# Kernel optimization log

Measured on AMD Instinct MI355X. Metric: run time of the kernel, lower is better.

Reference implementation:

```python
import jax, jax.numpy as jnp
import numpy as np

# Uniform-scope sizes: B molecules, A atoms/mol, G fragments/mol, W map width,
# H hidden, L attention layers, S = G+1 (fg prompt row prepended per molecule)
B, A, G, W, H, L = 1024, 64, 31, 8, 512, 2
S = G + 1
DK = 32  # attention head dim (hard-coded in the module)


def _layernorm(x, g, b, eps):
    mu = jnp.mean(x, axis=-1, keepdims=True)
    var = jnp.var(x, axis=-1, keepdims=True)
    return g * (x - mu) * jax.lax.rsqrt(var + eps) + b


def setup_inputs() -> dict:
    key = jax.random.key(0)
    ks = jax.random.split(key, 16)
    s = 0.02
    return {
        "f_atom": jax.random.normal(ks[0], (B * A, H), jnp.float32),
        "f_group": jax.random.normal(ks[1], (B * G, H), jnp.float32),
        "fg": jax.random.normal(ks[2], (1, 3 * H), jnp.float32),
        "alpha": 0.1 * jnp.ones((1,), jnp.float32),
        "lr_w": jax.random.normal(ks[3], (3 * H, H), jnp.float32) * s,
        "lr_b": jnp.zeros((H,), jnp.float32),
        "wq_w": jax.random.normal(ks[4], (L, H, DK), jnp.float32) * s,
        "wq_b": jnp.zeros((L, DK), jnp.float32),
        "wk_w": jax.random.normal(ks[5], (L, H, DK), jnp.float32) * s,
        "wk_b": jnp.zeros((L, DK), jnp.float32),
        "wv_w": jax.random.normal(ks[6], (L, H, DK), jnp.float32) * s,
        "wv_b": jnp.zeros((L, DK), jnp.float32),
        "dense_w": jax.random.normal(ks[7], (L, DK, H), jnp.float32) * s,
        "dense_b": jnp.zeros((L, H), jnp.float32),
        "ln_g": jnp.ones((L, H), jnp.float32),
        "ln_b": jnp.zeros((L, H), jnp.float32),
        "lin_w": jax.random.normal(ks[8], (H, H), jnp.float32) * s,
        "lin_b": jnp.zeros((H,), jnp.float32),
        "norm_g": jnp.ones((H,), jnp.float32),
        "norm_b": jnp.zeros((H,), jnp.float32),
        "mapping": jax.random.randint(ks[9], (B * G, W), 0, A + 1, jnp.int64),
    }


def reference(f_atom, f_group, fg, alpha, lr_w, lr_b, wq_w, wq_b, wk_w, wk_b,
              wv_w, wv_b, dense_w, dense_b, ln_g, ln_b, lin_w, lin_b,
              norm_g, norm_b, mapping):
    # --- ragged gather + reduce + pad (vectorized: uniform scopes) ---
    a = f_atom.reshape(B, A, H)
    # prepend zero padding row per molecule (mapping index 0 -> zeros)
    a_pad = jnp.concatenate([jnp.zeros((B, 1, H), a.dtype), a], axis=1)  # [B,A+1,H]
    m = mapping.reshape(B, G, W)
    gathered = a_pad[jnp.arange(B)[:, None, None], m]  # [B,G,W,H]
    g = f_group.reshape(B, G, H)
    cur_g = jnp.concatenate(
        [gathered.sum(axis=2), gathered.max(axis=2), g], axis=-1)  # [B,G,3H]
    brics = jnp.concatenate(
        [jnp.broadcast_to(fg[None], (B, 1, 3 * H)), cur_g], axis=1)  # [B,S,3H]

    f_frag = jax.nn.relu(brics @ lr_w + lr_b)  # [B,S,H]

    # mask built from init_hiddens = f_frag (same for every layer)
    pm = (f_frag != 0).astype(f_frag.dtype)
    mask = jnp.einsum('bsh,bth->bst', pm, pm)  # [B,S,S]
    neg = jnp.asarray(-1e9, f_frag.dtype)
    scale = 1.0 / np.sqrt(DK)

    hs = f_frag
    attn = None
    for l in range(L):
        q = hs @ wq_w[l] + wq_b[l]
        k = hs @ wk_w[l] + wk_b[l]
        v = hs @ wv_w[l] + wv_b[l]
        scores = jnp.einsum('bsd,btd->bst', q, k) * scale
        scores = jnp.where(mask == 0, neg, scores)
        attn = jax.nn.softmax(scores, axis=-1)
        x = jnp.einsum('bst,btd->bsd', attn, v)
        dh = x @ dense_w[l] + dense_b[l]  # dropout is identity in eval
        hs = _layernorm(dh + hs, ln_g[l], ln_b[l], 1e-6)

    f_out = _layernorm(hs @ lin_w + lin_b, norm_g, norm_b, 1e-5) * alpha[0]
    return f_out[:, 0, :], attn
```

## Files before the change

### kernel.cpp

```cpp
#include <hip/hip_runtime.h>

#define B_   1024
#define A_   64
#define G_   31
#define W_   8
#define H_   512
#define L_   2
#define S_   32
#define DK_  32
#define K3H_ 1536

typedef short short8 __attribute__((ext_vector_type(8)));
typedef float floatx4 __attribute__((ext_vector_type(4)));

__device__ __forceinline__ float bf2f(unsigned short u){
  union { unsigned int i; float f; } x; x.i = ((unsigned int)u) << 16; return x.f;
}
__device__ __forceinline__ unsigned short f2bf(float f){
  union { float f; unsigned int i; } x; x.f = f;
  unsigned int u = x.i;
  return (unsigned short)((u + 0x7FFFu + ((u >> 16) & 1u)) >> 16);
}
__device__ __forceinline__ void gl_lds16(const unsigned short* g, unsigned short* l){
  __builtin_amdgcn_global_load_lds((const __attribute__((address_space(1))) unsigned int*)g,
                                   (__attribute__((address_space(3))) unsigned int*)l, 16, 0, 0);
}

__global__ __launch_bounds__(256) void prep_weights(
    const float* __restrict__ lr_w, const float* __restrict__ wq_w, const float* __restrict__ wk_w,
    const float* __restrict__ wv_w, const float* __restrict__ dense_w, const float* __restrict__ lin_w,
    unsigned short* __restrict__ lr_wT, unsigned short* __restrict__ qkvT,
    unsigned short* __restrict__ denseT, unsigned short* __restrict__ lin_wT){
  int i = blockIdx.x * 256 + threadIdx.x;
  if (i < 786432){
    int n = i / K3H_, k = i % K3H_;
    lr_wT[i] = f2bf(lr_w[(size_t)k * H_ + n]);
    return;
  }
  i -= 786432;
  if (i < 98304){
    int k = i & 511; int t = i >> 9; int n = t & 31; int u = t >> 5;
    int p = u % 3, l = u / 3;
    const float* src = (p == 0) ? wq_w : (p == 1) ? wk_w : wv_w;
    qkvT[((size_t)((l*3+p)*S_ + n)) * H_ + k] = f2bf(src[((size_t)(l*H_ + k)) * DK_ + n]);
    return;
  }
  i -= 98304;
  if (i < 32768){
    int k = i & 31; int t = i >> 5; int n = t & 511; int l = t >> 9;
    denseT[((size_t)(l*H_ + n)) * DK_ + k] = f2bf(dense_w[((size_t)(l*DK_ + k)) * H_ + n]);
    return;
  }
  i -= 32768;
  int n = i >> 9, k = i & 511;
  lin_wT[(size_t)n * H_ + k] = f2bf(lin_w[(size_t)k * H_ + n]);
}

__global__ __launch_bounds__(64) void build_brics(
    const float* __restrict__ f_atom, const float* __restrict__ f_group,
    const float* __restrict__ fg, const int* __restrict__ mapping,
    unsigned short* __restrict__ brics){
  int blk = blockIdx.x;
  int b = blk >> 5, s = blk & 31;
  int t = threadIdx.x;
  unsigned short* out = brics + (size_t)blk * K3H_;
  if (s == 0){
    for (int k = t; k < K3H_; k += 64) out[k] = f2bf(fg[k]);
    return;
  }
  int g = s - 1;
  const int* mp = mapping + ((size_t)(b * G_ + g)) * W_;
  int c0 = t * 8;
  float sum[8], mx[8];
  #pragma unroll
  for (int j = 0; j < 8; ++j){ sum[j] = 0.f; mx[j] = -3.4e38f; }
  for (int w = 0; w < W_; ++w){
    int idx = mp[w];
    if (idx == 0){
      #pragma unroll
      for (int j = 0; j < 8; ++j) mx[j] = fmaxf(mx[j], 0.f);
    } else {
      const float* row = f_atom + ((size_t)(b * A_ + idx - 1)) * H_ + c0;
      float4 v0 = *(const float4*)row;
      float4 v1 = *(const float4*)(row + 4);
      float v[8] = {v0.x,v0.y,v0.z,v0.w,v1.x,v1.y,v1.z,v1.w};
      #pragma unroll
      for (int j = 0; j < 8; ++j){ sum[j] += v[j]; mx[j] = fmaxf(mx[j], v[j]); }
    }
  }
  const float* grow = f_group + ((size_t)(b * G_ + g)) * H_ + c0;
  float4 g0 = *(const float4*)grow;
  float4 g1 = *(const float4*)(grow + 4);
  float gv[8] = {g0.x,g0.y,g0.z,g0.w,g1.x,g1.y,g1.z,g1.w};
  unsigned short tmp[8] __attribute__((aligned(16)));
  #pragma unroll
  for (int j = 0; j < 8; ++j) tmp[j] = f2bf(sum[j]);
  *(uint4*)(out + c0) = *(const uint4*)tmp;
  #pragma unroll
  for (int j = 0; j < 8; ++j) tmp[j] = f2bf(mx[j]);
  *(uint4*)(out + 512 + c0) = *(const uint4*)tmp;
  #pragma unroll
  for (int j = 0; j < 8; ++j) tmp[j] = f2bf(gv[j]);
  *(uint4*)(out + 1024 + c0) = *(const uint4*)tmp;
}

__global__ __launch_bounds__(256) void gemm_frag(
    const unsigned short* __restrict__ brics, const unsigned short* __restrict__ wT,
    const float* __restrict__ lr_b, unsigned short* __restrict__ f_frag){
  __shared__ __align__(16) unsigned short As[128*32];
  __shared__ __align__(16) unsigned short Bs[128*32];
  int tid = threadIdx.x;
  int bx = blockIdx.x;
  int mtile = bx >> 2, ntile = bx & 3;
  int rowStart = mtile * 128, colStart = ntile * 128;
  int lane = tid & 63, wave = tid >> 6;
  int m16 = lane & 15, quad = lane >> 4;
  int wm = wave >> 1, wn = wave & 1;
  floatx4 acc[4][4];
  #pragma unroll
  for (int i = 0; i < 4; ++i)
    #pragma unroll
    for (int j = 0; j < 4; ++j) acc[i][j] = (floatx4){0.f,0.f,0.f,0.f};

  int r0 = tid >> 2, c0 = tid & 3;
  int r1 = (tid + 256) >> 2;
  for (int kt = 0; kt < K3H_/32; ++kt){
    const unsigned short* gA0 = brics + (size_t)(rowStart + r0) * K3H_ + kt*32 + c0*8;
    const unsigned short* gA1 = brics + (size_t)(rowStart + r1) * K3H_ + kt*32 + c0*8;
    const unsigned short* gB0 = wT + (size_t)(colStart + r0) * K3H_ + kt*32 + c0*8;
    const unsigned short* gB1 = wT + (size_t)(colStart + r1) * K3H_ + kt*32 + c0*8;
    gl_lds16(gA0, As + (size_t)tid * 8);
    gl_lds16(gA1, As + (size_t)(tid + 256) * 8);
    gl_lds16(gB0, Bs + (size_t)tid * 8);
    gl_lds16(gB1, Bs + (size_t)(tid + 256) * 8);
    __syncthreads();
    short8 af[4], bfr[4];
    #pragma unroll
    for (int i = 0; i < 4; ++i){
      af[i]  = *(const short8*)(As + ((wm*64 + i*16 + m16)*32 + quad*8));
      bfr[i] = *(const short8*)(Bs + ((wn*64 + i*16 + m16)*32 + quad*8));
    }
    #pragma unroll
    for (int i = 0; i < 4; ++i)
      #pragma unroll
      for (int j = 0; j < 4; ++j)
        acc[i][j] = __builtin_amdgcn_mfma_f32_16x16x32_bf16(af[i], bfr[j], acc[i][j], 0, 0, 0);
    __syncthreads();
  }
  #pragma unroll
  for (int i = 0; i < 4; ++i)
    #pragma unroll
    for (int j = 0; j < 4; ++j){
      int col = colStart + wn*64 + j*16 + m16;
      float bias = lr_b[col];
      #pragma unroll
      for (int r = 0; r < 4; ++r){
        int row = rowStart + wm*64 + i*16 + quad*4 + r;
        float v = acc[i][j][r] + bias;
        v = v > 0.f ? v : 0.f;
        f_frag[(size_t)row * H_ + col] = f2bf(v);
      }
    }
}

__global__ __launch_bounds__(256) void attn_kernel(
    const unsigned short* __restrict__ f_frag,
    const unsigned short* __restrict__ qkvT, const unsigned short* __restrict__ denseT,
    const float* __restrict__ wq_b, const float* __restrict__ wk_b, const float* __restrict__ wv_b,
    const float* __restrict__ dense_b, const float* __restrict__ ln_g, const float* __restrict__ ln_b,
    unsigned short* __restrict__ hsf, float* __restrict__ out_attn){
  const int HP = 544, TP = 40;
  __shared__ __align__(16) unsigned short hs[S_*544];
  __shared__ __align__(16) unsigned short Qs[S_*40];
  __shared__ __align__(16) unsigned short Ks[S_*40];
  __shared__ __align__(16) unsigned short Vt[S_*40];
  __shared__ __align__(16) unsigned short Ps[S_*40];
  __shared__ __align__(16) unsigned short Xs[S_*40];
  __shared__ unsigned long long pmask[S_*8];
  __shared__ unsigned int mz[S_];
  int b = blockIdx.x;
  int tid = threadIdx.x;
  int wave = tid >> 6, lane = tid & 63;
  int m16 = lane & 15, quad = lane >> 4;

  {
    int row = tid >> 3, cc = (tid & 7) * 64;
    const unsigned short* src = f_frag + ((size_t)(b * S_ + row)) * H_ + cc;
    unsigned short* dst = hs + row * HP + cc;
    #pragma unroll
    for (int k = 0; k < 64; k += 8)
      *(uint4*)(dst + k) = *(const uint4*)(src + k);
  }
  if (tid < S_) mz[tid] = 0u;
  __syncthreads();
  {
    int s = tid >> 3, w = tid & 7;
    unsigned long long m = 0ull;
    const unsigned short* hrow = hs + s * HP + w * 64;
    for (int j = 0; j < 64; ++j)
      if (hrow[j] != 0) m |= (1ull << j);
    pmask[s * 8 + w] = m;
  }
  __syncthreads();
  for (int idx = tid; idx < S_*S_; idx += 256){
    int s = idx >> 5, t2 = idx & 31;
    bool inter = false;
    #pragma unroll
    for (int w = 0; w < 8; ++w)
      inter = inter || ((pmask[s*8+w] & pmask[t2*8+w]) != 0ull);
    if (!inter) atomicOr(&mz[s], 1u << t2);
  }
  __syncthreads();

  const float scale = 0.17677669529663687f;
  for (int l = 0; l < L_; ++l){
    {
      int mt = wave >> 1, nt = wave & 1;
      floatx4 aq = {0,0,0,0}, ak = {0,0,0,0}, av = {0,0,0,0};
      const unsigned short* arow = hs + (mt*16 + m16) * HP + quad*8;
      const unsigned short* bq = qkvT + ((size_t)((l*3 + 0)*S_ + nt*16 + m16)) * H_ + quad*8;
      const unsigned short* bk = bq + (size_t)S_ * H_;
      const unsigned short* bv = bk + (size_t)S_ * H_;
      for (int k0 = 0; k0 < H_; k0 += 32){
        short8 a = *(const short8*)(arow + k0);
        aq = __builtin_amdgcn_mfma_f32_16x16x32_bf16(a, *(const short8*)(bq + k0), aq, 0,0,0);
        ak = __builtin_amdgcn_mfma_f32_16x16x32_bf16(a, *(const short8*)(bk + k0), ak, 0,0,0);
        av = __builtin_amdgcn_mfma_f32_16x16x32_bf16(a, *(const short8*)(bv + k0), av, 0,0,0);
      }
      int col = nt*16 + m16;
      float bqs = wq_b[l*DK_ + col], bks = wk_b[l*DK_ + col], bvs = wv_b[l*DK_ + col];
      #pragma unroll
      for (int r = 0; r < 4; ++r){
        int rw = mt*16 + quad*4 + r;
        Qs[rw*TP + col] = f2bf((aq[r] + bqs) * scale);
        Ks[rw*TP + col] = f2bf(ak[r] + bks);
        Vt[col*TP + rw] = f2bf(av[r] + bvs);
      }
    }
    __syncthreads();
    if (wave < 2){
      int mt = wave;
      short8 a  = *(const short8*)(Qs + (mt*16 + m16)*TP + quad*8);
      short8 b0 = *(const short8*)(Ks + m16*TP + quad*8);
      short8 b1 = *(const short8*)(Ks + (16 + m16)*TP + quad*8);
      floatx4 z = {0,0,0,0};
      floatx4 s0 = __builtin_amdgcn_mfma_f32_16x16x32_bf16(a, b0, z, 0,0,0);
      floatx4 s1 = __builtin_amdgcn_mfma_f32_16x16x32_bf16(a, b1, z, 0,0,0);
      #pragma unroll
      for (int r = 0; r < 4; ++r){
        int s = mt*16 + quad*4 + r;
        unsigned int m = mz[s];
        float v0 = ((m >> m16) & 1u) ? -1e9f : s0[r];
        float v1 = ((m >> (16 + m16)) & 1u) ? -1e9f : s1[r];
        float mx = fmaxf(v0, v1);
        #pragma unroll
        for (int d = 1; d < 16; d <<= 1) mx = fmaxf(mx, __shfl_xor(mx, d));
        float e0 = __expf(v0 - mx), e1 = __expf(v1 - mx);
        float sm = e0 + e1;
        #pragma unroll
        for (int d = 1; d < 16; d <<= 1) sm += __shfl_xor(sm, d);
        float inv = 1.f / sm;
        float p0 = e0 * inv, p1 = e1 * inv;
        Ps[s*TP + m16] = f2bf(p0);
        Ps[s*TP + 16 + m16] = f2bf(p1);
        if (l == L_ - 1){
          float* oa = out_attn + ((size_t)b * S_ + s) * S_;
          oa[m16] = p0; oa[16 + m16] = p1;
        }
      }
    }
    __syncthreads();
    {
      int mt = wave >> 1, nt = wave & 1;
      short8 a  = *(const short8*)(Ps + (mt*16 + m16)*TP + quad*8);
      short8 bv = *(const short8*)(Vt + (nt*16 + m16)*TP + quad*8);
      floatx4 z = {0,0,0,0};
      floatx4 x = __builtin_amdgcn_mfma_f32_16x16x32_bf16(a, bv, z, 0,0,0);
      #pragma unroll
      for (int r = 0; r < 4; ++r)
        Xs[(mt*16 + quad*4 + r)*TP + nt*16 + m16] = f2bf(x[r]);
    }
    __syncthreads();
    {
      short8 ax0 = *(const short8*)(Xs + m16*TP + quad*8);
      short8 ax1 = *(const short8*)(Xs + (16 + m16)*TP + quad*8);
      #pragma unroll
      for (int j = 0; j < 8; ++j){
        int col = (wave*8 + j)*16 + m16;
        short8 bw = *(const short8*)(denseT + ((size_t)(l*H_ + col)) * DK_ + quad*8);
        float db = dense_b[l*H_ + col];
        floatx4 z = {0,0,0,0};
        floatx4 d0 = __builtin_amdgcn_mfma_f32_16x16x32_bf16(ax0, bw, z, 0,0,0);
        floatx4 d1 = __builtin_amdgcn_mfma_f32_16x16x32_bf16(ax1, bw, z, 0,0,0);
        #pragma unroll
        for (int r = 0; r < 4; ++r){
          int row0 = quad*4 + r;
          float y0 = d0[r] + db + bf2f(hs[row0*HP + col]);
          hs[row0*HP + col] = f2bf(y0);
          int row1 = 16 + quad*4 + r;
          float y1 = d1[r] + db + bf2f(hs[row1*HP + col]);
          hs[row1*HP + col] = f2bf(y1);
        }
      }
    }
    __syncthreads();
    {
      #pragma unroll
      for (int rr = 0; rr < 8; ++rr){
        int row = wave*8 + rr;
        unsigned short* hrow = hs + row*HP + lane*8;
        short8 hv = *(const short8*)hrow;
        float v[8]; float s1 = 0.f, s2 = 0.f;
        #pragma unroll
        for (int j = 0; j < 8; ++j){ v[j] = bf2f((unsigned short)hv[j]); s1 += v[j]; s2 += v[j]*v[j]; }
        #pragma unroll
        for (int d = 1; d < 64; d <<= 1){ s1 += __shfl_xor(s1, d); s2 += __shfl_xor(s2, d); }
        float mean = s1 * (1.f/512.f);
        float var = s2 * (1.f/512.f) - mean*mean;
        float rs = rsqrtf(var + 1e-6f);
        unsigned short o[8] __attribute__((aligned(16)));
        #pragma unroll
        for (int j = 0; j < 8; ++j){
          int colj = lane*8 + j;
          float nv = (v[j] - mean) * rs * ln_g[l*H_ + colj] + ln_b[l*H_ + colj];
          o[j] = f2bf(nv);
        }
        *(uint4*)hrow = *(const uint4*)o;
      }
    }
    __syncthreads();
  }
  if (tid < 64){
    *(uint4*)(hsf + (size_t)b * H_ + tid*8) = *(const uint4*)(hs + tid*8);
  }
}

__global__ __launch_bounds__(256) void final_kernel(
    const unsigned short* __restrict__ hsf, const unsigned short* __restrict__ lin_wT,
    const float* __restrict__ lin_b, const float* __restrict__ norm_g, const float* __restrict__ norm_b,
    const float* __restrict__ alpha, float* __restrict__ out_f){
  const int HP = 544;
  __shared__ __align__(16) unsigned short hsb[32*544];
  int blk = blockIdx.x;
  int tid = threadIdx.x;
  int wave = tid >> 6, lane = tid & 63;
  int m16 = lane & 15, quad = lane >> 4;
  {
    int row = tid >> 3, cc = (tid & 7) * 64;
    const unsigned short* src = hsf + ((size_t)(blk*32 + row)) * H_ + cc;
    unsigned short* dst = hsb + row*HP + cc;
    #pragma unroll
    for (int k = 0; k < 64; k += 8)
      *(uint4*)(dst + k) = *(const uint4*)(src + k);
  }
  __syncthreads();
  floatx4 acc[2][8];
  #pragma unroll
  for (int mt = 0; mt < 2; ++mt)
    #pragma unroll
    for (int j = 0; j < 8; ++j) acc[mt][j] = (floatx4){0.f,0.f,0.f,0.f};
  for (int k0 = 0; k0 < H_; k0 += 32){
    short8 a0 = *(const short8*)(hsb + m16*HP + k0 + quad*8);
    short8 a1 = *(const short8*)(hsb + (16 + m16)*HP + k0 + quad*8);
    #pragma unroll
    for (int j = 0; j < 8; ++j){
      int n = (wave*8 + j)*16 + m16;
      short8 bw = *(const short8*)(lin_wT + (size_t)n * H_ + k0 + quad*8);
      acc[0][j] = __builtin_amdgcn_mfma_f32_16x16x32_bf16(a0, bw, acc[0][j], 0,0,0);
      acc[1][j] = __builtin_amdgcn_mfma_f32_16x16x32_bf16(a1, bw, acc[1][j], 0,0,0);
    }
  }
  __syncthreads();
  #pragma unroll
  for (int mt = 0; mt < 2; ++mt)
    #pragma unroll
    for (int j = 0; j < 8; ++j){
      int col = (wave*8 + j)*16 + m16;
      float lb = lin_b[col];
      #pragma unroll
      for (int r = 0; r < 4; ++r){
        int row = mt*16 + quad*4 + r;
        hsb[row*HP + col] = f2bf(acc[mt][j][r] + lb);
      }
    }
  __syncthreads();
  float al = alpha[0];
  #pragma unroll
  for (int rr = 0; rr < 8; ++rr){
    int row = wave*8 + rr;
    const unsigned short* hrow = hsb + row*HP + lane*8;
    short8 hv = *(const short8*)hrow;
    float v[8]; float s1 = 0.f, s2 = 0.f;
    #pragma unroll
    for (int j = 0; j < 8; ++j){ v[j] = bf2f((unsigned short)hv[j]); s1 += v[j]; s2 += v[j]*v[j]; }
    #pragma unroll
    for (int d = 1; d < 64; d <<= 1){ s1 += __shfl_xor(s1, d); s2 += __shfl_xor(s2, d); }
    float mean = s1 * (1.f/512.f);
    float var = s2 * (1.f/512.f) - mean*mean;
    float rs = rsqrtf(var + 1e-5f);
    float o[8];
    #pragma unroll
    for (int j = 0; j < 8; ++j){
      int colj = lane*8 + j;
      o[j] = ((v[j] - mean) * rs * norm_g[colj] + norm_b[colj]) * al;
    }
    float* op = out_f + ((size_t)(blk*32 + row)) * H_ + lane*8;
    float4 f0 = {o[0], o[1], o[2], o[3]};
    float4 f1 = {o[4], o[5], o[6], o[7]};
    *(float4*)op = f0;
    *(float4*)(op + 4) = f1;
  }
}

extern "C" void kernel_launch(void* const* d_in, const int* in_sizes, int n_in,
                              void* d_out, int out_size, void* d_ws, size_t ws_size,
                              hipStream_t stream){
  const float* f_atom  = (const float*)d_in[0];
  const float* f_group = (const float*)d_in[1];
  const float* fg      = (const float*)d_in[2];
  const float* alpha   = (const float*)d_in[3];
  const float* lr_w    = (const float*)d_in[4];
  const float* lr_b    = (const float*)d_in[5];
  const float* wq_w    = (const float*)d_in[6];
  const float* wq_b    = (const float*)d_in[7];
  const float* wk_w    = (const float*)d_in[8];
  const float* wk_b    = (const float*)d_in[9];
  const float* wv_w    = (const float*)d_in[10];
  const float* wv_b    = (const float*)d_in[11];
  const float* dense_w = (const float*)d_in[12];
  const float* dense_b = (const float*)d_in[13];
  const float* ln_g    = (const float*)d_in[14];
  const float* ln_b    = (const float*)d_in[15];
  const float* lin_w   = (const float*)d_in[16];
  const float* lin_b   = (const float*)d_in[17];
  const float* norm_g  = (const float*)d_in[18];
  const float* norm_b  = (const float*)d_in[19];
  const int*   mapping = (const int*)d_in[20];

  unsigned short* brics  = (unsigned short*)d_ws;
  unsigned short* f_frag = brics  + (size_t)32768 * 1536;
  unsigned short* lr_wT  = f_frag + (size_t)32768 * 512;
  unsigned short* qkvT   = lr_wT  + (size_t)512 * 1536;
  unsigned short* denseT = qkvT   + (size_t)2*3*32*512;
  unsigned short* lin_wT = denseT + (size_t)2*512*32;
  unsigned short* hsf    = lin_wT + (size_t)512*512;

  float* out_f    = (float*)d_out;
  float* out_attn = out_f + (size_t)B_ * H_;

  prep_weights<<<4608, 256, 0, stream>>>(lr_w, wq_w, wk_w, wv_w, dense_w, lin_w,
                                         lr_wT, qkvT, denseT, lin_wT);
  build_brics<<<B_ * S_, 64, 0, stream>>>(f_atom, f_group, fg, mapping, brics);
  gemm_frag<<<(32768/128) * (512/128), 256, 0, stream>>>(brics, lr_wT, lr_b, f_frag);
  attn_kernel<<<B_, 256, 0, stream>>>(f_frag, qkvT, denseT, wq_b, wk_b, wv_b,
                                      dense_b, ln_g, ln_b, hsf, out_attn);
  final_kernel<<<B_/32, 256, 0, stream>>>(hsf, lin_wT, lin_b, norm_g, norm_b, alpha, out_f);
}
```

Baseline: 514.5 us.

## Tile weight transposes, widen brics blocks, and swizzle gemm_frag LDS with K=64

Splits weight prep into an LDS-tiled transpose kernel for the large lr_w/lin_w matrices, which gives coalesced reads and writes, and a small kernel for the qkv/dense weights. build_brics now packs four (molecule, row) pairs into one 256-thread block. gemm_frag doubles its K step to 64 with an XOR-swizzled LDS layout to avoid bank conflicts and halve the number of barriers. It also remaps block IDs so that blocks sharing an M tile land on the same XCD for L2 reuse. The cost is more LDS per block, which could lower occupancy.

```diff
diff --git a/kernel.cpp b/kernel.cpp
--- a/kernel.cpp
+++ b/kernel.cpp
@@ -26,18 +26,41 @@
                                    (__attribute__((address_space(3))) unsigned int*)l, 16, 0, 0);
 }
 
-__global__ __launch_bounds__(256) void prep_weights(
-    const float* __restrict__ lr_w, const float* __restrict__ wq_w, const float* __restrict__ wk_w,
-    const float* __restrict__ wv_w, const float* __restrict__ dense_w, const float* __restrict__ lin_w,
-    unsigned short* __restrict__ lr_wT, unsigned short* __restrict__ qkvT,
-    unsigned short* __restrict__ denseT, unsigned short* __restrict__ lin_wT){
+__global__ __launch_bounds__(256) void prep_transpose(
+    const float* __restrict__ lr_w, const float* __restrict__ lin_w,
+    unsigned short* __restrict__ lr_wT, unsigned short* __restrict__ lin_wT){
+  __shared__ float tile[64][65];
+  int bx = blockIdx.x;
+  const float* src; unsigned short* dst; int R, C;
+  if (bx < 192){ src = lr_w;  dst = lr_wT;  R = 1536; C = 512; }
+  else         { bx -= 192; src = lin_w; dst = lin_wT; R = 512;  C = 512; }
+  int rt = bx >> 3, ct = bx & 7;
+  int tid = threadIdx.x;
+  int r16 = tid >> 4, c4 = tid & 15;
+  #pragma unroll
+  for (int p = 0; p < 4; ++p){
+    int row = p*16 + r16;
+    float4 v = *(const float4*)(src + (size_t)(rt*64 + row) * C + ct*64 + c4*4);
+    tile[row][c4*4+0] = v.x; tile[row][c4*4+1] = v.y;
+    tile[row][c4*4+2] = v.z; tile[row][c4*4+3] = v.w;
+  }
+  __syncthreads();
+  int rr = tid >> 3, cc8 = tid & 7;
+  #pragma unroll
+  for (int p = 0; p < 2; ++p){
+    int n = p*32 + rr;
+    unsigned short o[8] __attribute__((aligned(16)));
+    #pragma unroll
+    for (int j = 0; j < 8; ++j) o[j] = f2bf(tile[cc8*8 + j][n]);
+    *(uint4*)(dst + (size_t)(ct*64 + n) * R + rt*64 + cc8*8) = *(const uint4*)o;
+  }
+}
+
+__global__ __launch_bounds__(256) void prep_small(
+    const float* __restrict__ wq_w, const float* __restrict__ wk_w, const float* __restrict__ wv_w,
+    const float* __restrict__ dense_w,
+    unsigned short* __restrict__ qkvT, unsigned short* __restrict__ denseT){
   int i = blockIdx.x * 256 + threadIdx.x;
-  if (i < 786432){
-    int n = i / K3H_, k = i % K3H_;
-    lr_wT[i] = f2bf(lr_w[(size_t)k * H_ + n]);
-    return;
-  }
-  i -= 786432;
   if (i < 98304){
     int k = i & 511; int t = i >> 9; int n = t & 31; int u = t >> 5;
     int p = u % 3, l = u / 3;
@@ -46,24 +69,18 @@
     return;
   }
   i -= 98304;
-  if (i < 32768){
-    int k = i & 31; int t = i >> 5; int n = t & 511; int l = t >> 9;
-    denseT[((size_t)(l*H_ + n)) * DK_ + k] = f2bf(dense_w[((size_t)(l*DK_ + k)) * H_ + n]);
-    return;
-  }
-  i -= 32768;
-  int n = i >> 9, k = i & 511;
-  lin_wT[(size_t)n * H_ + k] = f2bf(lin_w[(size_t)k * H_ + n]);
-}
-
-__global__ __launch_bounds__(64) void build_brics(
+  int k = i & 31; int t = i >> 5; int n = t & 511; int l = t >> 9;
+  denseT[((size_t)(l*H_ + n)) * DK_ + k] = f2bf(dense_w[((size_t)(l*DK_ + k)) * H_ + n]);
+}
+
+__global__ __launch_bounds__(256) void build_brics(
     const float* __restrict__ f_atom, const float* __restrict__ f_group,
     const float* __restrict__ fg, const int* __restrict__ mapping,
     unsigned short* __restrict__ brics){
-  int blk = blockIdx.x;
-  int b = blk >> 5, s = blk & 31;
-  int t = threadIdx.x;
-  unsigned short* out = brics + (size_t)blk * K3H_;
+  int pair = blockIdx.x * 4 + (threadIdx.x >> 6);
+  int b = pair >> 5, s = pair & 31;
+  int t = threadIdx.x & 63;
+  unsigned short* out = brics + (size_t)pair * K3H_;
   if (s == 0){
     for (int k = t; k < K3H_; k += 64) out[k] = f2bf(fg[k]);
     return;
@@ -107,11 +124,13 @@
 __global__ __launch_bounds__(256) void gemm_frag(
     const unsigned short* __restrict__ brics, const unsigned short* __restrict__ wT,
     const float* __restrict__ lr_b, unsigned short* __restrict__ f_frag){
-  __shared__ __align__(16) unsigned short As[128*32];
-  __shared__ __align__(16) unsigned short Bs[128*32];
+  __shared__ __align__(16) unsigned short As[128*64];
+  __shared__ __align__(16) unsigned short Bs[128*64];
   int tid = threadIdx.x;
   int bx = blockIdx.x;
-  int mtile = bx >> 2, ntile = bx & 3;
+  int xcd = bx & 7, slot = bx >> 3;
+  int mtile = xcd + 8 * (slot >> 2);
+  int ntile = slot & 3;
   int rowStart = mtile * 128, colStart = ntile * 128;
   int lane = tid & 63, wave = tid >> 6;
   int m16 = lane & 15, quad = lane >> 4;
@@ -122,29 +141,40 @@
     #pragma unroll
     for (int j = 0; j < 4; ++j) acc[i][j] = (floatx4){0.f,0.f,0.f,0.f};
 
-  int r0 = tid >> 2, c0 = tid & 3;
-  int r1 = (tid + 256) >> 2;
-  for (int kt = 0; kt < K3H_/32; ++kt){
-    const unsigned short* gA0 = brics + (size_t)(rowStart + r0) * K3H_ + kt*32 + c0*8;
-    const unsigned short* gA1 = brics + (size_t)(rowStart + r1) * K3H_ + kt*32 + c0*8;
-    const unsigned short* gB0 = wT + (size_t)(colStart + r0) * K3H_ + kt*32 + c0*8;
-    const unsigned short* gB1 = wT + (size_t)(colStart + r1) * K3H_ + kt*32 + c0*8;
-    gl_lds16(gA0, As + (size_t)tid * 8);
-    gl_lds16(gA1, As + (size_t)(tid + 256) * 8);
-    gl_lds16(gB0, Bs + (size_t)tid * 8);
-    gl_lds16(gB1, Bs + (size_t)(tid + 256) * 8);
-    __syncthreads();
-    short8 af[4], bfr[4];
-    #pragma unroll
-    for (int i = 0; i < 4; ++i){
-      af[i]  = *(const short8*)(As + ((wm*64 + i*16 + m16)*32 + quad*8));
-      bfr[i] = *(const short8*)(Bs + ((wn*64 + i*16 + m16)*32 + quad*8));
-    }
-    #pragma unroll
-    for (int i = 0; i < 4; ++i)
-      #pragma unroll
-      for (int j = 0; j < 4; ++j)
-        acc[i][j] = __builtin_amdgcn_mfma_f32_16x16x32_bf16(af[i], bfr[j], acc[i][j], 0, 0, 0);
+  int srow = tid >> 3;
+  int gchunk = (tid & 7) ^ (srow & 7);
+  size_t aOff[4], bOff[4];
+  #pragma unroll
+  for (int p = 0; p < 4; ++p){
+    aOff[p] = (size_t)(rowStart + p*32 + srow) * K3H_ + gchunk*8;
+    bOff[p] = (size_t)(colStart + p*32 + srow) * K3H_ + gchunk*8;
+  }
+  int fsw0 = ((0*4 + quad) ^ (m16 & 7)) * 8;
+  int fsw1 = ((1*4 + quad) ^ (m16 & 7)) * 8;
+
+  for (int kt = 0; kt < K3H_/64; ++kt){
+    int kbase = kt * 64;
+    #pragma unroll
+    for (int p = 0; p < 4; ++p){
+      gl_lds16(brics + aOff[p] + kbase, As + p*2048 + (size_t)tid*8);
+      gl_lds16(wT    + bOff[p] + kbase, Bs + p*2048 + (size_t)tid*8);
+    }
+    __syncthreads();
+    #pragma unroll
+    for (int ks = 0; ks < 2; ++ks){
+      int fsw = ks ? fsw1 : fsw0;
+      short8 af[4], bfr[4];
+      #pragma unroll
+      for (int i = 0; i < 4; ++i){
+        af[i]  = *(const short8*)(As + (wm*64 + i*16 + m16)*64 + fsw);
+        bfr[i] = *(const short8*)(Bs + (wn*64 + i*16 + m16)*64 + fsw);
+      }
+      #pragma unroll
+      for (int i = 0; i < 4; ++i)
+        #pragma unroll
+        for (int j = 0; j < 4; ++j)
+          acc[i][j] = __builtin_amdgcn_mfma_f32_16x16x32_bf16(af[i], bfr[j], acc[i][j], 0, 0, 0);
+    }
     __syncthreads();
   }
   #pragma unroll
@@ -448,9 +478,9 @@
   float* out_f    = (float*)d_out;
   float* out_attn = out_f + (size_t)B_ * H_;
 
-  prep_weights<<<4608, 256, 0, stream>>>(lr_w, wq_w, wk_w, wv_w, dense_w, lin_w,
-                                         lr_wT, qkvT, denseT, lin_wT);
-  build_brics<<<B_ * S_, 64, 0, stream>>>(f_atom, f_group, fg, mapping, brics);
+  prep_transpose<<<256, 256, 0, stream>>>(lr_w, lin_w, lr_wT, lin_wT);
+  prep_small<<<512, 256, 0, stream>>>(wq_w, wk_w, wv_w, dense_w, qkvT, denseT);
+  build_brics<<<B_ * S_ / 4, 256, 0, stream>>>(f_atom, f_group, fg, mapping, brics);
   gemm_frag<<<(32768/128) * (512/128), 256, 0, stream>>>(brics, lr_wT, lr_b, f_frag);
   attn_kernel<<<B_, 256, 0, stream>>>(f_frag, qkvT, denseT, wq_b, wk_b, wv_b,
                                       dense_b, ln_g, ln_b, hsf, out_attn);
```

New measurement: 502.6 us. 2.3% less time.
